# Kernel tuning notes

Measured on AMD Instinct MI355X. Metric: run time of the kernel, lower is better.

The kernel has to match this reference:

```python
import jax, jax.numpy as jnp
import numpy as np

B, IN_C, H, W = 2, 256, 128, 128
KQ = 128            # kq_dim
K_LOCAL = 5         # subsample_local_ksize -> 25 local samples
S = 32              # subsample_num_samples (25 local + 7 random global)
STRIDES = (1, 2, 4) # levels 2, 3, 4


def _local_inds(h, w, k):
    # create_local_ind_buffer: flat index of the KxK window around each pixel,
    # coordinates clamped at the border (padding by replication).
    off = np.arange(k) - k // 2
    ii = np.clip(np.arange(h)[:, None] + off[None, :], 0, h - 1)  # [h,k]
    jj = np.clip(np.arange(w)[:, None] + off[None, :], 0, w - 1)  # [w,k]
    inds = ii[:, None, :, None] * w + jj[None, :, None, :]        # [h,w,k,k]
    return inds.reshape(h * w, k * k)


def setup_inputs() -> dict:
    key = jax.random.key(0)
    ks = jax.random.split(key, 4)
    rng = np.random.RandomState(0)
    inp = {
        'feats': jax.random.normal(ks[0], (B, IN_C, H, W), jnp.float32),
        'conv_w': jax.random.normal(ks[1], (KQ, IN_C, 3, 3), jnp.float32) * 0.02,
        'conv_b': jnp.zeros((KQ,), jnp.float32),
        'key_w': jax.random.normal(ks[2], (KQ, KQ), jnp.float32) * 0.05,
        'key_b': jnp.zeros((KQ,), jnp.float32),
        'query_w': jax.random.normal(ks[3], (KQ, KQ), jnp.float32) * 0.05,
        'query_b': jnp.zeros((KQ,), jnp.float32),
    }
    for lvl, s in zip((2, 3, 4), STRIDES):
        h, w = H // s, W // s
        n = h * w
        loc = np.broadcast_to(_local_inds(h, w, K_LOCAL)[None], (B, n, K_LOCAL * K_LOCAL))
        glob = rng.randint(0, n, size=(B, n, S - K_LOCAL * K_LOCAL))
        inp['sample_inds_%d' % lvl] = jnp.asarray(np.concatenate([loc, glob], -1), jnp.int32)
    return inp


def _pool(x, s):
    # utils.downscale_tensor: average-pool by the level stride
    if s == 1:
        return x
    b, c, h, w = x.shape
    return x.reshape(b, c, h // s, s, w // s, s).mean(axis=(3, 5))


def _level_logits(key_f, query_f, stride, inds):
    k = _pool(key_f, stride)
    q = _pool(query_f, stride)
    b, c, h, w = k.shape
    k = k.reshape(b, c, h * w).transpose(0, 2, 1)   # [B,N,C]
    q = q.reshape(b, c, h * w).transpose(0, 2, 1)   # [B,N,C]
    gk = k[jnp.arange(b)[:, None, None], inds]      # gather keys -> [B,N,S,C]
    # (gathered_query * gathered_key).sum(-1); query gather at node_inds is identity
    return jnp.einsum('bnc,bnsc->bns', q, gk) * (c ** -0.5)


def reference(feats, conv_w, conv_b, key_w, key_b, query_w, query_b,
              sample_inds_2, sample_inds_3, sample_inds_4):
    x = jax.lax.conv_general_dilated(
        feats, conv_w, (1, 1), 'SAME',
        dimension_numbers=('NCHW', 'OIHW', 'NCHW')) + conv_b[None, :, None, None]
    keys = jnp.einsum('bchw,kc->bkhw', x, key_w) + key_b[None, :, None, None]
    queries = jnp.einsum('bchw,kc->bkhw', x, query_w) + query_b[None, :, None, None]
    logits = [
        _level_logits(keys, queries, s, i)
        for s, i in zip(STRIDES, (sample_inds_2, sample_inds_3, sample_inds_4))
    ]
    # subsample_logits for levels 2/3/4, concatenated along the node dim
    return jnp.concatenate(logits, axis=1)  # [B, 16384+4096+1024, S]
```

## Files before the change

kernel.cpp:

```cpp
#include <hip/hip_runtime.h>
#include <cstddef>
#include <cstdint>

typedef __attribute__((ext_vector_type(8))) short short8;
typedef __attribute__((ext_vector_type(4))) float f32x4;

namespace {
constexpr int B_   = 2;
constexpr int HW   = 16384;
constexpr int NTOT = 21504;
constexpr float SCALE = 0.088388347648318447f;
}

__device__ __forceinline__ unsigned short f2bf(float f) {
    unsigned u = __builtin_bit_cast(unsigned, f);
    u += 0x7fffu + ((u >> 16) & 1u);
    return (unsigned short)(u >> 16);
}
__device__ __forceinline__ float bf2f(unsigned short h) {
    return __builtin_bit_cast(float, (unsigned)h << 16);
}
__device__ __forceinline__ float blo(unsigned u) {
    return __builtin_bit_cast(float, u << 16);
}
__device__ __forceinline__ float bhi(unsigned u) {
    return __builtin_bit_cast(float, u & 0xffff0000u);
}
__device__ __forceinline__ unsigned pk2(float a, float b) {
    return (unsigned)f2bf(a) | ((unsigned)f2bf(b) << 16);
}
__device__ __forceinline__ void gload_lds16(const void* g, void* l) {
    __builtin_amdgcn_global_load_lds(
        (const __attribute__((address_space(1))) void*)g,
        (__attribute__((address_space(3))) void*)l, 16, 0, 0);
}

__global__ __launch_bounds__(256) void tp_k(
    const float* __restrict__ feats, const float* __restrict__ cw,
    const float* __restrict__ kw, const float* __restrict__ qw,
    const float* __restrict__ cb, const float* __restrict__ kb,
    const float* __restrict__ qb, unsigned short* __restrict__ fpm,
    unsigned short* __restrict__ wp, float* __restrict__ bias)
{
    const int bid = blockIdx.x;
    const int tid = threadIdx.x;

    if (bid < 520) {
        const int b = bid >= 260;
        const int rem = bid - b * 260;
        const int y = rem >> 1, xseg = rem & 1;
        const int lane = tid & 63, cg = tid >> 6;
        const int x = (xseg << 6) + lane;
        const bool inter = (y >= 1 && y <= 128);
        const float* src = feats + (((size_t)b * 256) << 14) + ((y - 1) << 7) + x;
        unsigned short* orow = fpm + ((size_t)(b * 130 + y) * 130 + 1 + x) * 256;

#pragma unroll
        for (int it = 0; it < 8; ++it) {
            const int c0 = (it << 5) + (cg << 3);
            uint4 v = {0u, 0u, 0u, 0u};
            if (inter) {
                float f0 = src[(size_t)(c0 + 0) << 14], f1 = src[(size_t)(c0 + 1) << 14];
                float f2 = src[(size_t)(c0 + 2) << 14], f3 = src[(size_t)(c0 + 3) << 14];
                float f4 = src[(size_t)(c0 + 4) << 14], f5 = src[(size_t)(c0 + 5) << 14];
                float f6 = src[(size_t)(c0 + 6) << 14], f7 = src[(size_t)(c0 + 7) << 14];
                v.x = pk2(f0, f1); v.y = pk2(f2, f3); v.z = pk2(f4, f5); v.w = pk2(f6, f7);
            }
            *(uint4*)(orow + c0) = v;
        }
        if (xseg == 0) {
            uint4 z = {0u, 0u, 0u, 0u};
            if (tid < 32)
                *(uint4*)(fpm + ((size_t)(b * 130 + y) * 130 + 0) * 256 + (tid << 3)) = z;
            else if (tid < 64)
                *(uint4*)(fpm + ((size_t)(b * 130 + y) * 130 + 129) * 256 + ((tid - 32) << 3)) = z;
        }
        return;
    }

    if (bid == 1096) {
        __shared__ float cbv[128];
        if (tid < 128) cbv[tid] = cb[tid];
        __syncthreads();
        const int oc = tid & 127, isQ = tid >> 7;
        const float* wrow = (isQ ? qw : kw) + oc * 128;
        float a = isQ ? qb[oc] : kb[oc];
        for (int j = 0; j < 128; ++j) a += wrow[j] * cbv[j];
        bias[tid] = a;
        return;
    }

    __shared__ float cvec[128][4];
    const int g = bid - 520;
    for (int idx = tid; idx < 512; idx += 256) {
        int j = idx >> 2, q = idx & 3;
        int pair = (g << 2) + q;
        int c = pair / 9, tap = pair - c * 9;
        cvec[j][q] = cw[j * 2304 + c * 9 + tap];
    }
    __syncthreads();
    const int oc = tid & 127, isQ = tid >> 7;
    const float* wrow = (isQ ? qw : kw) + oc * 128;
    float acc0 = 0.f, acc1 = 0.f, acc2 = 0.f, acc3 = 0.f;
    for (int j = 0; j < 128; ++j) {
        float wv = wrow[j];
        acc0 += wv * cvec[j][0]; acc1 += wv * cvec[j][1];
        acc2 += wv * cvec[j][2]; acc3 += wv * cvec[j][3];
    }
    float accs[4] = {acc0, acc1, acc2, acc3};
#pragma unroll
    for (int q = 0; q < 4; ++q) {
        int pair = (g << 2) + q;
        int c = pair / 9, tap = pair - c * 9;
        int chunk = c >> 5, kg = (c >> 3) & 3, i = c & 7;
        int nf = (isQ << 3) + (oc >> 4);
        int lane = (kg << 4) + (oc & 15);
        wp[((size_t)(((chunk * 9 + tap) << 4) + nf) << 9) + (lane << 3) + i] = f2bf(accs[q]);
    }
}

__global__ __launch_bounds__(256, 2) void conv3_k(
    const unsigned short* __restrict__ fpm, const unsigned short* __restrict__ wp,
    const float* __restrict__ kqbias, unsigned short* __restrict__ kT,
    unsigned short* __restrict__ qT, unsigned short* __restrict__ kT2,
    unsigned short* __restrict__ qT2, unsigned short* __restrict__ kT3,
    unsigned short* __restrict__ qT3)
{
    __shared__ __align__(16) unsigned char abuf[2][7168];
    __shared__ __align__(16) unsigned short obuf[64 * 264];

    const int tid = threadIdx.x;
    const int w = tid >> 6, lane = tid & 63;
    const int bid = blockIdx.x;
    const int b = bid >> 8, tile = bid & 255;
    const int ty0 = (tile >> 4) << 3, tx0 = (tile & 15) << 3;
    const int r = lane & 15, g = lane >> 4;

    const int sp_sub = lane >> 2, sp_o = (lane & 3) << 4;
    const int pbase = (((r >> 3) * 10) + (r & 7)) * 64 + (g << 4);
    const unsigned char* wpB = (const unsigned char*)wp + ((w << 2) << 10) + (lane << 4);

    f32x4 acc[4][4];
#pragma unroll
    for (int mi = 0; mi < 4; ++mi)
#pragma unroll
        for (int ni = 0; ni < 4; ++ni) acc[mi][ni] = (f32x4){0.f, 0.f, 0.f, 0.f};

    auto stage = [&](int chunk, int buf) {
#pragma unroll
        for (int k = 0; k < 2; ++k) {
            int i = w + (k << 2);
            if (i < 7) {
                int pl0 = (i << 4) + sp_sub;
                int y = (pl0 * 6554) >> 16;
                int x = pl0 - y * 10;
                const unsigned char* src = (const unsigned char*)fpm +
                    (((size_t)((b * 130 + ty0 + y) * 130 + tx0 + x)) << 9) +
                    (chunk << 6) + sp_o;
                gload_lds16(src, &abuf[buf][i << 10]);
            }
        }
    };

    stage(0, 0);
    __syncthreads();

    for (int chunk = 0; chunk < 8; ++chunk) {
        const unsigned char* ab = abuf[chunk & 1];
        if (chunk < 7) stage(chunk + 1, (chunk + 1) & 1);
        const unsigned char* wbase = wpB + (size_t)chunk * 147456;
#pragma unroll
        for (int tap = 0; tap < 9; ++tap) {
            const int dy = tap / 3, dx = tap % 3;
            short8 bf[4];
#pragma unroll
            for (int ni = 0; ni < 4; ++ni)
                bf[ni] = *(const short8*)(wbase + tap * 16384 + (ni << 10));
            short8 af[4];
#pragma unroll
            for (int mi = 0; mi < 4; ++mi)
                af[mi] = *(const short8*)(ab + pbase + (((2 * mi + dy) * 10 + dx) << 6));
#pragma unroll
            for (int mi = 0; mi < 4; ++mi)
#pragma unroll
                for (int ni = 0; ni < 4; ++ni)
                    acc[mi][ni] = __builtin_amdgcn_mfma_f32_16x16x32_bf16(
                        af[mi], bf[ni], acc[mi][ni], 0, 0, 0);
        }
        __syncthreads();
    }

    const int col = lane & 15;
    const int mrow0 = g << 2;
#pragma unroll
    for (int ni = 0; ni < 4; ++ni) {
        const int nf = (w << 2) + ni;
        const float bv = kqbias[(nf << 4) + col];
#pragma unroll
        for (int mi = 0; mi < 4; ++mi)
#pragma unroll
            for (int reg = 0; reg < 4; ++reg) {
                int m = mrow0 + reg;
                int pxl = ((2 * mi + (m >> 3)) << 3) + (m & 7);
                obuf[pxl * 264 + (nf << 4) + col] = f2bf(acc[mi][ni][reg] + bv);
            }
    }
    __syncthreads();

    {
        const int px = tid >> 2, q = tid & 3;
        const int gp = ((ty0 + (px >> 3)) << 7) + tx0 + (px & 7);
        const unsigned short* srow = obuf + px * 264 + (q << 6);
        unsigned short* dp = (q < 2)
            ? kT + ((((size_t)b << 14) + gp) << 7) + (q << 6)
            : qT + ((((size_t)b << 14) + gp) << 7) + ((q - 2) << 6);
#pragma unroll
        for (int j = 0; j < 8; ++j)
            *(uint4*)(dp + (j << 3)) = *(const uint4*)(srow + (j << 3));
    }

    {
        const int pp = tid >> 4, ocg = tid & 15, oc0 = ocg << 4;
        const int py2 = pp >> 2, px2 = pp & 3;
        const int gp2 = (((ty0 >> 1) + py2) << 6) + (tx0 >> 1) + px2;
        unsigned short* dp = (oc0 < 128)
            ? kT2 + (((size_t)b * 4096 + gp2) << 7) + oc0
            : qT2 + (((size_t)b * 4096 + gp2) << 7) + (oc0 - 128);
#pragma unroll
        for (int h = 0; h < 2; ++h) {
            float s0=0,s1=0,s2=0,s3=0,s4=0,s5=0,s6=0,s7=0;
#pragma unroll
            for (int dy = 0; dy < 2; ++dy)
#pragma unroll
                for (int dx = 0; dx < 2; ++dx) {
                    int pxl = (((py2 << 1) + dy) << 3) + (px2 << 1) + dx;
                    uint4 v = *(const uint4*)(obuf + pxl * 264 + oc0 + (h << 3));
                    s0 += blo(v.x); s1 += bhi(v.x); s2 += blo(v.y); s3 += bhi(v.y);
                    s4 += blo(v.z); s5 += bhi(v.z); s6 += blo(v.w); s7 += bhi(v.w);
                }
            uint4 o;
            o.x = pk2(s0 * 0.25f, s1 * 0.25f); o.y = pk2(s2 * 0.25f, s3 * 0.25f);
            o.z = pk2(s4 * 0.25f, s5 * 0.25f); o.w = pk2(s6 * 0.25f, s7 * 0.25f);
            *(uint4*)(dp + (h << 3)) = o;
        }
    }

    if (tid < 64) {
        const int pp = tid >> 4, ocg = tid & 15, oc0 = ocg << 4;
        const int py4 = pp >> 1, px4 = pp & 1;
        const int gp4 = (((ty0 >> 2) + py4) << 5) + (tx0 >> 2) + px4;
        unsigned short* dp = (oc0 < 128)
            ? kT3 + (((size_t)b * 1024 + gp4) << 7) + oc0
            : qT3 + (((size_t)b * 1024 + gp4) << 7) + (oc0 - 128);
#pragma unroll
        for (int h = 0; h < 2; ++h) {
            float s0=0,s1=0,s2=0,s3=0,s4=0,s5=0,s6=0,s7=0;
#pragma unroll
            for (int dy = 0; dy < 4; ++dy)
#pragma unroll
                for (int dx = 0; dx < 4; ++dx) {
                    int pxl = (((py4 << 2) + dy) << 3) + (px4 << 2) + dx;
                    uint4 v = *(const uint4*)(obuf + pxl * 264 + oc0 + (h << 3));
                    s0 += blo(v.x); s1 += bhi(v.x); s2 += blo(v.y); s3 += bhi(v.y);
                    s4 += blo(v.z); s5 += bhi(v.z); s6 += blo(v.w); s7 += bhi(v.w);
                }
            const float f = 0.0625f;
            uint4 o;
            o.x = pk2(s0 * f, s1 * f); o.y = pk2(s2 * f, s3 * f);
            o.z = pk2(s4 * f, s5 * f); o.w = pk2(s6 * f, s7 * f);
            *(uint4*)(dp + (h << 3)) = o;
        }
    }
}

__global__ __launch_bounds__(512) void gdot_all_k(
    const unsigned short* __restrict__ qT1, const unsigned short* __restrict__ kT1,
    const unsigned short* __restrict__ qT2, const unsigned short* __restrict__ kT2,
    const unsigned short* __restrict__ qT3, const unsigned short* __restrict__ kT3,
    const int* __restrict__ i2, const int* __restrict__ i3, const int* __restrict__ i4,
    float* __restrict__ out)
{
    __shared__ __align__(16) unsigned char kwin[144 * 256];

    const int raw = blockIdx.x;
    const int bid = (raw & 7) * 84 + (raw >> 3);

    const unsigned short *qT, *kT;
    const int* inds;
    int n, wshift, tpbsh, twsh, off;
    if (bid < 512) {
        qT = qT1; kT = kT1; inds = i2; n = 16384; wshift = 7; tpbsh = 8; twsh = 4; off = 0;
    } else if (bid < 640) {
        qT = qT2; kT = kT2; inds = i3; n = 4096;  wshift = 6; tpbsh = 6; twsh = 3; off = 16384;
    } else {
        qT = qT3; kT = kT3; inds = i4; n = 1024;  wshift = 5; tpbsh = 4; twsh = 2; off = 20480;
    }
    const int lb   = bid - ((bid < 512) ? 0 : (bid < 640) ? 512 : 640);
    const int b    = lb >> tpbsh;
    const int tile = lb & ((1 << tpbsh) - 1);
    const int ty0  = (tile >> twsh) << 3;
    const int tx0  = (tile & ((1 << twsh) - 1)) << 3;
    const int W    = 1 << wshift, Wm1 = W - 1;
    const int ry0  = ty0 - 2, cx0 = tx0 - 2;

    const int tid   = threadIdx.x;
    const int pxl   = tid >> 3;
    const int slice = tid & 7;
    const int py = pxl >> 3, px = pxl & 7;
    const int nid = ((ty0 + py) << wshift) + tx0 + px;

    for (int idx = tid; idx < 2304; idx += 512) {
        int slot = idx >> 4, w16 = idx & 15;
        int sy = ry0 + slot / 12, sx = cx0 + slot % 12;
        sy = min(max(sy, 0), Wm1); sx = min(max(sx, 0), Wm1);
        uint4 v = *(const uint4*)(kT + ((size_t)(b * n + (sy << wshift) + sx) * 128) + (w16 << 3));
        *(uint4*)&kwin[slot * 256 + ((w16 ^ (slot & 7)) << 4)] = v;
    }

    float qr[16];
    {
        const uint4* qp = (const uint4*)(qT + ((size_t)(b * n + nid) * 128) + (slice << 4));
        uint4 q0 = qp[0], q1 = qp[1];
        qr[0] = blo(q0.x); qr[1] = bhi(q0.x); qr[2] = blo(q0.y); qr[3] = bhi(q0.y);
        qr[4] = blo(q0.z); qr[5] = bhi(q0.z); qr[6] = blo(q0.w); qr[7] = bhi(q0.w);
        qr[8] = blo(q1.x); qr[9] = bhi(q1.x); qr[10] = blo(q1.y); qr[11] = bhi(q1.y);
        qr[12] = blo(q1.z); qr[13] = bhi(q1.z); qr[14] = blo(q1.w); qr[15] = bhi(q1.w);
    }
    __syncthreads();

    const int* irow = inds + ((size_t)(b * n + nid) << 5);
    int ia[32];
    {
        const int4* ip = (const int4*)irow;
#pragma unroll
        for (int j = 0; j < 8; ++j) {
            int4 v = ip[j];
            ia[4 * j] = v.x; ia[4 * j + 1] = v.y; ia[4 * j + 2] = v.z; ia[4 * j + 3] = v.w;
        }
    }

    uint4 rk0[7], rk1[7];
#pragma unroll
    for (int rr = 0; rr < 7; ++rr) {
        const uint4* kp = (const uint4*)(kT + (((size_t)(b * n + ia[25 + rr])) << 7) + (slice << 4));
        rk0[rr] = kp[0]; rk1[rr] = kp[1];
    }

    const int w2 = slice << 1;
    float res4[4] = {0.f, 0.f, 0.f, 0.f};
    float* orow = out + (((size_t)b * NTOT + off + nid) << 5);

#pragma unroll
    for (int s = 0; s < 32; ++s) {
        uint4 k0, k1;
        if (s < 25) {
            int ind = ia[s];
            int iy = ind >> wshift, ix = ind & Wm1;
            int slot = (iy - ry0) * 12 + (ix - cx0);
            int sw = slot & 7;
            const unsigned char* base2 = kwin + slot * 256;
            k0 = *(const uint4*)(base2 + ((w2 ^ sw) << 4));
            k1 = *(const uint4*)(base2 + (((w2 + 1) ^ sw) << 4));
        } else {
            k0 = rk0[s - 25]; k1 = rk1[s - 25];
        }
        float a = qr[0] * blo(k0.x) + qr[1] * bhi(k0.x)
                + qr[2] * blo(k0.y) + qr[3] * bhi(k0.y)
                + qr[4] * blo(k0.z) + qr[5] * bhi(k0.z)
                + qr[6] * blo(k0.w) + qr[7] * bhi(k0.w)
                + qr[8] * blo(k1.x) + qr[9] * bhi(k1.x)
                + qr[10] * blo(k1.y) + qr[11] * bhi(k1.y)
                + qr[12] * blo(k1.z) + qr[13] * bhi(k1.z)
                + qr[14] * blo(k1.w) + qr[15] * bhi(k1.w);
        a += __shfl_xor(a, 1);
        a += __shfl_xor(a, 2);
        a += __shfl_xor(a, 4);
        if ((s >> 2) == slice) res4[s & 3] = a * SCALE;
    }
    *(float4*)(orow + (slice << 2)) = *(const float4*)res4;
}

extern "C" void kernel_launch(void* const* d_in, const int* in_sizes, int n_in,
                              void* d_out, int out_size, void* d_ws, size_t ws_size,
                              hipStream_t stream)
{
    const float* feats = (const float*)d_in[0];
    const float* cw    = (const float*)d_in[1];
    const float* cb    = (const float*)d_in[2];
    const float* kw    = (const float*)d_in[3];
    const float* kb    = (const float*)d_in[4];
    const float* qw    = (const float*)d_in[5];
    const float* qb    = (const float*)d_in[6];
    const int*   i2    = (const int*)d_in[7];
    const int*   i3    = (const int*)d_in[8];
    const int*   i4    = (const int*)d_in[9];
    float* out = (float*)d_out;

    char* ws = (char*)d_ws;
    unsigned short* wp   = (unsigned short*)ws;
    float*          bias = (float*)(ws + 1179648);
    unsigned short* fpm  = (unsigned short*)(ws + 1180672);
    unsigned short* kT1  = (unsigned short*)(ws + 18624512);
    unsigned short* qT1  = kT1 + 4194304;
    unsigned short* kT2  = qT1 + 4194304;
    unsigned short* qT2  = kT2 + 1048576;
    unsigned short* kT3  = qT2 + 1048576;
    unsigned short* qT3  = kT3 + 262144;

    tp_k<<<dim3(1097), 256, 0, stream>>>(feats, cw, kw, qw, cb, kb, qb,
                                         fpm, wp, bias);
    conv3_k<<<dim3(512), 256, 0, stream>>>(fpm, wp, bias, kT1, qT1,
                                           kT2, qT2, kT3, qT3);
    gdot_all_k<<<dim3(672), 512, 0, stream>>>(qT1, kT1, qT2, kT2, qT3, kT3,
                                              i2, i3, i4, out);
}
```

Before: 181.2 us.

## Fuse three kernels into one cooperative persistent kernel with grid syncs

Merges the transpose/weight-prep, conv and gather-dot kernels into one cooperative kernel of 512 blocks that calls grid.sync() between phases. The aim is to remove launch gaps and inter-kernel drains. The gather-dot phase is also reworked from 512 to 256 threads, so each thread covers 32 channels and the random global keys are loaded inside the loop rather than prefetched. The costs are grid-sync overhead, occupancy limited to what a co-resident grid allows, and a less parallel gdot phase. If the cooperative launch fails, it falls back to three separate kernels.

```diff
diff --git a/kernel.cpp b/kernel.cpp
--- a/kernel.cpp
+++ b/kernel.cpp
@@ -1,6 +1,9 @@
 #include <hip/hip_runtime.h>
+#include <hip/hip_cooperative_groups.h>
 #include <cstddef>
 #include <cstdint>
+
+namespace cg = cooperative_groups;
 
 typedef __attribute__((ext_vector_type(8))) short short8;
 typedef __attribute__((ext_vector_type(4))) float f32x4;
@@ -35,21 +38,20 @@
         (__attribute__((address_space(3))) void*)l, 16, 0, 0);
 }
 
-__global__ __launch_bounds__(256) void tp_k(
+__device__ __forceinline__ void phase_tp(
+    int v, int tid,
     const float* __restrict__ feats, const float* __restrict__ cw,
     const float* __restrict__ kw, const float* __restrict__ qw,
     const float* __restrict__ cb, const float* __restrict__ kb,
     const float* __restrict__ qb, unsigned short* __restrict__ fpm,
-    unsigned short* __restrict__ wp, float* __restrict__ bias)
-{
-    const int bid = blockIdx.x;
-    const int tid = threadIdx.x;
-
-    if (bid < 520) {
-        const int b = bid >= 260;
-        const int rem = bid - b * 260;
+    unsigned short* __restrict__ wp, float* __restrict__ bias,
+    float* fsm)
+{
+    if (v < 520) {
+        const int b = v >= 260;
+        const int rem = v - b * 260;
         const int y = rem >> 1, xseg = rem & 1;
-        const int lane = tid & 63, cg = tid >> 6;
+        const int lane = tid & 63, cg2 = tid >> 6;
         const int x = (xseg << 6) + lane;
         const bool inter = (y >= 1 && y <= 128);
         const float* src = feats + (((size_t)b * 256) << 14) + ((y - 1) << 7) + x;
@@ -57,16 +59,16 @@
 
 #pragma unroll
         for (int it = 0; it < 8; ++it) {
-            const int c0 = (it << 5) + (cg << 3);
-            uint4 v = {0u, 0u, 0u, 0u};
+            const int c0 = (it << 5) + (cg2 << 3);
+            uint4 w = {0u, 0u, 0u, 0u};
             if (inter) {
                 float f0 = src[(size_t)(c0 + 0) << 14], f1 = src[(size_t)(c0 + 1) << 14];
                 float f2 = src[(size_t)(c0 + 2) << 14], f3 = src[(size_t)(c0 + 3) << 14];
                 float f4 = src[(size_t)(c0 + 4) << 14], f5 = src[(size_t)(c0 + 5) << 14];
                 float f6 = src[(size_t)(c0 + 6) << 14], f7 = src[(size_t)(c0 + 7) << 14];
-                v.x = pk2(f0, f1); v.y = pk2(f2, f3); v.z = pk2(f4, f5); v.w = pk2(f6, f7);
+                w.x = pk2(f0, f1); w.y = pk2(f2, f3); w.z = pk2(f4, f5); w.w = pk2(f6, f7);
             }
-            *(uint4*)(orow + c0) = v;
+            *(uint4*)(orow + c0) = w;
         }
         if (xseg == 0) {
             uint4 z = {0u, 0u, 0u, 0u};
@@ -78,8 +80,8 @@
         return;
     }
 
-    if (bid == 1096) {
-        __shared__ float cbv[128];
+    if (v == 1096) {
+        float* cbv = fsm;
         if (tid < 128) cbv[tid] = cb[tid];
         __syncthreads();
         const int oc = tid & 127, isQ = tid >> 7;
@@ -87,11 +89,12 @@
         float a = isQ ? qb[oc] : kb[oc];
         for (int j = 0; j < 128; ++j) a += wrow[j] * cbv[j];
         bias[tid] = a;
+        __syncthreads();
         return;
     }
 
-    __shared__ float cvec[128][4];
-    const int g = bid - 520;
+    float (*cvec)[4] = (float(*)[4])fsm;
+    const int g = v - 520;
     for (int idx = tid; idx < 512; idx += 256) {
         int j = idx >> 2, q = idx & 3;
         int pair = (g << 2) + q;
@@ -101,13 +104,13 @@
     __syncthreads();
     const int oc = tid & 127, isQ = tid >> 7;
     const float* wrow = (isQ ? qw : kw) + oc * 128;
-    float acc0 = 0.f, acc1 = 0.f, acc2 = 0.f, acc3 = 0.f;
+    float a0 = 0.f, a1 = 0.f, a2 = 0.f, a3 = 0.f;
     for (int j = 0; j < 128; ++j) {
         float wv = wrow[j];
-        acc0 += wv * cvec[j][0]; acc1 += wv * cvec[j][1];
-        acc2 += wv * cvec[j][2]; acc3 += wv * cvec[j][3];
-    }
-    float accs[4] = {acc0, acc1, acc2, acc3};
+        a0 += wv * cvec[j][0]; a1 += wv * cvec[j][1];
+        a2 += wv * cvec[j][2]; a3 += wv * cvec[j][3];
+    }
+    float accs[4] = {a0, a1, a2, a3};
 #pragma unroll
     for (int q = 0; q < 4; ++q) {
         int pair = (g << 2) + q;
@@ -117,21 +120,20 @@
         int lane = (kg << 4) + (oc & 15);
         wp[((size_t)(((chunk * 9 + tap) << 4) + nf) << 9) + (lane << 3) + i] = f2bf(accs[q]);
     }
-}
-
-__global__ __launch_bounds__(256, 2) void conv3_k(
+    __syncthreads();
+}
+
+__device__ __forceinline__ void phase_conv(
+    int bid, int tid,
     const unsigned short* __restrict__ fpm, const unsigned short* __restrict__ wp,
     const float* __restrict__ kqbias, unsigned short* __restrict__ kT,
     unsigned short* __restrict__ qT, unsigned short* __restrict__ kT2,
     unsigned short* __restrict__ qT2, unsigned short* __restrict__ kT3,
-    unsigned short* __restrict__ qT3)
-{
-    __shared__ __align__(16) unsigned char abuf[2][7168];
-    __shared__ __align__(16) unsigned short obuf[64 * 264];
-
-    const int tid = threadIdx.x;
+    unsigned short* __restrict__ qT3, unsigned char* smem)
+{
+    unsigned short* obuf = (unsigned short*)(smem + 14336);
+
     const int w = tid >> 6, lane = tid & 63;
-    const int bid = blockIdx.x;
     const int b = bid >> 8, tile = bid & 255;
     const int ty0 = (tile >> 4) << 3, tx0 = (tile & 15) << 3;
     const int r = lane & 15, g = lane >> 4;
@@ -157,7 +159,7 @@
                 const unsigned char* src = (const unsigned char*)fpm +
                     (((size_t)((b * 130 + ty0 + y) * 130 + tx0 + x)) << 9) +
                     (chunk << 6) + sp_o;
-                gload_lds16(src, &abuf[buf][i << 10]);
+                gload_lds16(src, smem + buf * 7168 + (i << 10));
             }
         }
     };
@@ -166,7 +168,7 @@
     __syncthreads();
 
     for (int chunk = 0; chunk < 8; ++chunk) {
-        const unsigned char* ab = abuf[chunk & 1];
+        const unsigned char* ab = smem + (chunk & 1) * 7168;
         if (chunk < 7) stage(chunk + 1, (chunk + 1) & 1);
         const unsigned char* wbase = wpB + (size_t)chunk * 147456;
 #pragma unroll
@@ -273,29 +275,25 @@
     }
 }
 
-__global__ __launch_bounds__(512) void gdot_all_k(
+__device__ __forceinline__ void phase_gdot(
+    int v, int tid,
     const unsigned short* __restrict__ qT1, const unsigned short* __restrict__ kT1,
     const unsigned short* __restrict__ qT2, const unsigned short* __restrict__ kT2,
     const unsigned short* __restrict__ qT3, const unsigned short* __restrict__ kT3,
     const int* __restrict__ i2, const int* __restrict__ i3, const int* __restrict__ i4,
-    float* __restrict__ out)
-{
-    __shared__ __align__(16) unsigned char kwin[144 * 256];
-
-    const int raw = blockIdx.x;
-    const int bid = (raw & 7) * 84 + (raw >> 3);
-
+    float* __restrict__ out, unsigned char* kwin)
+{
     const unsigned short *qT, *kT;
     const int* inds;
     int n, wshift, tpbsh, twsh, off;
-    if (bid < 512) {
+    if (v < 512) {
         qT = qT1; kT = kT1; inds = i2; n = 16384; wshift = 7; tpbsh = 8; twsh = 4; off = 0;
-    } else if (bid < 640) {
+    } else if (v < 640) {
         qT = qT2; kT = kT2; inds = i3; n = 4096;  wshift = 6; tpbsh = 6; twsh = 3; off = 16384;
     } else {
         qT = qT3; kT = kT3; inds = i4; n = 1024;  wshift = 5; tpbsh = 4; twsh = 2; off = 20480;
     }
-    const int lb   = bid - ((bid < 512) ? 0 : (bid < 640) ? 512 : 640);
+    const int lb   = v - ((v < 512) ? 0 : (v < 640) ? 512 : 640);
     const int b    = lb >> tpbsh;
     const int tile = lb & ((1 << tpbsh) - 1);
     const int ty0  = (tile >> twsh) << 3;
@@ -303,28 +301,31 @@
     const int W    = 1 << wshift, Wm1 = W - 1;
     const int ry0  = ty0 - 2, cx0 = tx0 - 2;
 
-    const int tid   = threadIdx.x;
-    const int pxl   = tid >> 3;
-    const int slice = tid & 7;
+    const int pxl = tid >> 2;
+    const int sl  = tid & 3;
     const int py = pxl >> 3, px = pxl & 7;
     const int nid = ((ty0 + py) << wshift) + tx0 + px;
 
-    for (int idx = tid; idx < 2304; idx += 512) {
+    for (int idx = tid; idx < 2304; idx += 256) {
         int slot = idx >> 4, w16 = idx & 15;
         int sy = ry0 + slot / 12, sx = cx0 + slot % 12;
         sy = min(max(sy, 0), Wm1); sx = min(max(sx, 0), Wm1);
-        uint4 v = *(const uint4*)(kT + ((size_t)(b * n + (sy << wshift) + sx) * 128) + (w16 << 3));
-        *(uint4*)&kwin[slot * 256 + ((w16 ^ (slot & 7)) << 4)] = v;
-    }
-
-    float qr[16];
+        uint4 vv = *(const uint4*)(kT + ((size_t)(b * n + (sy << wshift) + sx) << 7) + (w16 << 3));
+        *(uint4*)&kwin[slot * 256 + ((w16 ^ (slot & 7)) << 4)] = vv;
+    }
+
+    float qr[32];
     {
-        const uint4* qp = (const uint4*)(qT + ((size_t)(b * n + nid) * 128) + (slice << 4));
-        uint4 q0 = qp[0], q1 = qp[1];
-        qr[0] = blo(q0.x); qr[1] = bhi(q0.x); qr[2] = blo(q0.y); qr[3] = bhi(q0.y);
-        qr[4] = blo(q0.z); qr[5] = bhi(q0.z); qr[6] = blo(q0.w); qr[7] = bhi(q0.w);
-        qr[8] = blo(q1.x); qr[9] = bhi(q1.x); qr[10] = blo(q1.y); qr[11] = bhi(q1.y);
-        qr[12] = blo(q1.z); qr[13] = bhi(q1.z); qr[14] = blo(q1.w); qr[15] = bhi(q1.w);
+        const uint4* qp = (const uint4*)(qT + (((size_t)(b * n + nid)) << 7) + (sl << 5));
+        uint4 q0 = qp[0], q1 = qp[1], q2 = qp[2], q3 = qp[3];
+        qr[0]=blo(q0.x); qr[1]=bhi(q0.x); qr[2]=blo(q0.y); qr[3]=bhi(q0.y);
+        qr[4]=blo(q0.z); qr[5]=bhi(q0.z); qr[6]=blo(q0.w); qr[7]=bhi(q0.w);
+        qr[8]=blo(q1.x); qr[9]=bhi(q1.x); qr[10]=blo(q1.y); qr[11]=bhi(q1.y);
+        qr[12]=blo(q1.z); qr[13]=bhi(q1.z); qr[14]=blo(q1.w); qr[15]=bhi(q1.w);
+        qr[16]=blo(q2.x); qr[17]=bhi(q2.x); qr[18]=blo(q2.y); qr[19]=bhi(q2.y);
+        qr[20]=blo(q2.z); qr[21]=bhi(q2.z); qr[22]=blo(q2.w); qr[23]=bhi(q2.w);
+        qr[24]=blo(q3.x); qr[25]=bhi(q3.x); qr[26]=blo(q3.y); qr[27]=bhi(q3.y);
+        qr[28]=blo(q3.z); qr[29]=bhi(q3.z); qr[30]=blo(q3.w); qr[31]=bhi(q3.w);
     }
     __syncthreads();
 
@@ -334,50 +335,102 @@
         const int4* ip = (const int4*)irow;
 #pragma unroll
         for (int j = 0; j < 8; ++j) {
-            int4 v = ip[j];
-            ia[4 * j] = v.x; ia[4 * j + 1] = v.y; ia[4 * j + 2] = v.z; ia[4 * j + 3] = v.w;
-        }
-    }
-
-    uint4 rk0[7], rk1[7];
-#pragma unroll
-    for (int rr = 0; rr < 7; ++rr) {
-        const uint4* kp = (const uint4*)(kT + (((size_t)(b * n + ia[25 + rr])) << 7) + (slice << 4));
-        rk0[rr] = kp[0]; rk1[rr] = kp[1];
-    }
-
-    const int w2 = slice << 1;
-    float res4[4] = {0.f, 0.f, 0.f, 0.f};
+            int4 t = ip[j];
+            ia[4*j] = t.x; ia[4*j+1] = t.y; ia[4*j+2] = t.z; ia[4*j+3] = t.w;
+        }
+    }
+
+    const int w16b = sl << 2;
+    float res[8];
     float* orow = out + (((size_t)b * NTOT + off + nid) << 5);
 
 #pragma unroll
     for (int s = 0; s < 32; ++s) {
-        uint4 k0, k1;
+        uint4 k0, k1, k2, k3;
         if (s < 25) {
             int ind = ia[s];
             int iy = ind >> wshift, ix = ind & Wm1;
             int slot = (iy - ry0) * 12 + (ix - cx0);
             int sw = slot & 7;
             const unsigned char* base2 = kwin + slot * 256;
-            k0 = *(const uint4*)(base2 + ((w2 ^ sw) << 4));
-            k1 = *(const uint4*)(base2 + (((w2 + 1) ^ sw) << 4));
+            k0 = *(const uint4*)(base2 + (((w16b + 0) ^ sw) << 4));
+            k1 = *(const uint4*)(base2 + (((w16b + 1) ^ sw) << 4));
+            k2 = *(const uint4*)(base2 + (((w16b + 2) ^ sw) << 4));
+            k3 = *(const uint4*)(base2 + (((w16b + 3) ^ sw) << 4));
         } else {
-            k0 = rk0[s - 25]; k1 = rk1[s - 25];
-        }
-        float a = qr[0] * blo(k0.x) + qr[1] * bhi(k0.x)
-                + qr[2] * blo(k0.y) + qr[3] * bhi(k0.y)
-                + qr[4] * blo(k0.z) + qr[5] * bhi(k0.z)
-                + qr[6] * blo(k0.w) + qr[7] * bhi(k0.w)
-                + qr[8] * blo(k1.x) + qr[9] * bhi(k1.x)
-                + qr[10] * blo(k1.y) + qr[11] * bhi(k1.y)
-                + qr[12] * blo(k1.z) + qr[13] * bhi(k1.z)
-                + qr[14] * blo(k1.w) + qr[15] * bhi(k1.w);
+            const uint4* kp = (const uint4*)(kT + (((size_t)(b * n + ia[s])) << 7) + (sl << 5));
+            k0 = kp[0]; k1 = kp[1]; k2 = kp[2]; k3 = kp[3];
+        }
+        float a = qr[0]*blo(k0.x) + qr[1]*bhi(k0.x) + qr[2]*blo(k0.y) + qr[3]*bhi(k0.y)
+                + qr[4]*blo(k0.z) + qr[5]*bhi(k0.z) + qr[6]*blo(k0.w) + qr[7]*bhi(k0.w)
+                + qr[8]*blo(k1.x) + qr[9]*bhi(k1.x) + qr[10]*blo(k1.y) + qr[11]*bhi(k1.y)
+                + qr[12]*blo(k1.z) + qr[13]*bhi(k1.z) + qr[14]*blo(k1.w) + qr[15]*bhi(k1.w)
+                + qr[16]*blo(k2.x) + qr[17]*bhi(k2.x) + qr[18]*blo(k2.y) + qr[19]*bhi(k2.y)
+                + qr[20]*blo(k2.z) + qr[21]*bhi(k2.z) + qr[22]*blo(k2.w) + qr[23]*bhi(k2.w)
+                + qr[24]*blo(k3.x) + qr[25]*bhi(k3.x) + qr[26]*blo(k3.y) + qr[27]*bhi(k3.y)
+                + qr[28]*blo(k3.z) + qr[29]*bhi(k3.z) + qr[30]*blo(k3.w) + qr[31]*bhi(k3.w);
         a += __shfl_xor(a, 1);
         a += __shfl_xor(a, 2);
-        a += __shfl_xor(a, 4);
-        if ((s >> 2) == slice) res4[s & 3] = a * SCALE;
-    }
-    *(float4*)(orow + (slice << 2)) = *(const float4*)res4;
+        if ((s >> 3) == sl) res[s & 7] = a * SCALE;
+    }
+    float4 r0 = {res[0], res[1], res[2], res[3]};
+    float4 r1 = {res[4], res[5], res[6], res[7]};
+    *(float4*)(orow + (sl << 3)) = r0;
+    *(float4*)(orow + (sl << 3) + 4) = r1;
+    __syncthreads();
+}
+
+__global__ __launch_bounds__(256, 2) void fused_k(
+    const float* feats, const float* cw, const float* kw, const float* qw,
+    const float* cb, const float* kb, const float* qb,
+    unsigned short* fpm, unsigned short* wp, float* bias,
+    unsigned short* kT1, unsigned short* qT1, unsigned short* kT2,
+    unsigned short* qT2, unsigned short* kT3, unsigned short* qT3,
+    const int* i2, const int* i3, const int* i4, float* out)
+{
+    __shared__ __align__(16) unsigned char smem[48128];
+    const int tid = threadIdx.x;
+    cg::grid_group grid = cg::this_grid();
+
+    for (int v = blockIdx.x; v < 1097; v += 512)
+        phase_tp(v, tid, feats, cw, kw, qw, cb, kb, qb, fpm, wp, bias, (float*)smem);
+
+    grid.sync();
+
+    phase_conv(blockIdx.x, tid, fpm, wp, bias, kT1, qT1, kT2, qT2, kT3, qT3, smem);
+
+    grid.sync();
+
+    for (int v = blockIdx.x; v < 672; v += 512)
+        phase_gdot(v, tid, qT1, kT1, qT2, kT2, qT3, kT3, i2, i3, i4, out, smem);
+}
+
+__global__ __launch_bounds__(256) void tp_sep_k(
+    const float* feats, const float* cw, const float* kw, const float* qw,
+    const float* cb, const float* kb, const float* qb,
+    unsigned short* fpm, unsigned short* wp, float* bias)
+{
+    __shared__ __align__(16) float fsm[512];
+    phase_tp(blockIdx.x, threadIdx.x, feats, cw, kw, qw, cb, kb, qb, fpm, wp, bias, fsm);
+}
+
+__global__ __launch_bounds__(256, 2) void conv_sep_k(
+    const unsigned short* fpm, const unsigned short* wp, const float* kqbias,
+    unsigned short* kT1, unsigned short* qT1, unsigned short* kT2,
+    unsigned short* qT2, unsigned short* kT3, unsigned short* qT3)
+{
+    __shared__ __align__(16) unsigned char smem[48128];
+    phase_conv(blockIdx.x, threadIdx.x, fpm, wp, kqbias, kT1, qT1, kT2, qT2, kT3, qT3, smem);
+}
+
+__global__ __launch_bounds__(256) void gdot_sep_k(
+    const unsigned short* qT1, const unsigned short* kT1,
+    const unsigned short* qT2, const unsigned short* kT2,
+    const unsigned short* qT3, const unsigned short* kT3,
+    const int* i2, const int* i3, const int* i4, float* out)
+{
+    __shared__ __align__(16) unsigned char kwin[36864];
+    phase_gdot(blockIdx.x, threadIdx.x, qT1, kT1, qT2, kT2, qT3, kT3, i2, i3, i4, out, kwin);
 }
 
 extern "C" void kernel_launch(void* const* d_in, const int* in_sizes, int n_in,
@@ -407,10 +460,23 @@
     unsigned short* kT3  = qT2 + 1048576;
     unsigned short* qT3  = kT3 + 262144;
 
-    tp_k<<<dim3(1097), 256, 0, stream>>>(feats, cw, kw, qw, cb, kb, qb,
-                                         fpm, wp, bias);
-    conv3_k<<<dim3(512), 256, 0, stream>>>(fpm, wp, bias, kT1, qT1,
-                                           kT2, qT2, kT3, qT3);
-    gdot_all_k<<<dim3(672), 512, 0, stream>>>(qT1, kT1, qT2, kT2, qT3, kT3,
-                                              i2, i3, i4, out);
-}
+    void* args[] = {
+        (void*)&feats, (void*)&cw, (void*)&kw, (void*)&qw,
+        (void*)&cb, (void*)&kb, (void*)&qb,
+        (void*)&fpm, (void*)&wp, (void*)&bias,
+        (void*)&kT1, (void*)&qT1, (void*)&kT2, (void*)&qT2,
+        (void*)&kT3, (void*)&qT3,
+        (void*)&i2, (void*)&i3, (void*)&i4, (void*)&out
+    };
+    hipError_t err = hipLaunchCooperativeKernel(
+        (const void*)fused_k, dim3(512), dim3(256), args, 0, stream);
+
+    if (err != hipSuccess) {
+        tp_sep_k<<<dim3(1097), 256, 0, stream>>>(feats, cw, kw, qw, cb, kb, qb,
+                                                 fpm, wp, bias);
+        conv_sep_k<<<dim3(512), 256, 0, stream>>>(fpm, wp, bias, kT1, qT1,
+                                                  kT2, qT2, kT3, qT3);
+        gdot_sep_k<<<dim3(672), 256, 0, stream>>>(qT1, kT1, qT2, kT2, qT3, kT3,
+                                                  i2, i3, i4, out);
+    }
+}
```

After: 342.8 us. 1.89x slower.

## Split fused conv GEMM across output-channel halves to double block count

Applied to the files above, without the earlier changes.

The fused conv+key/query projection kernel is split so each block computes only the key or the query half (128 output channels) for its 8x8 pixel tile, launching 1024 blocks instead of 512. Per-wave accumulators halve, the output staging buffer shrinks, and the launch bound asks for 4 blocks per CU, all aimed at higher occupancy and better CU fill. In exchange, every input tile is staged from global memory twice, once per half.

```diff
diff --git a/kernel.cpp b/kernel.cpp
--- a/kernel.cpp
+++ b/kernel.cpp
@@ -101,13 +101,13 @@
     __syncthreads();
     const int oc = tid & 127, isQ = tid >> 7;
     const float* wrow = (isQ ? qw : kw) + oc * 128;
-    float acc0 = 0.f, acc1 = 0.f, acc2 = 0.f, acc3 = 0.f;
+    float a0 = 0.f, a1 = 0.f, a2 = 0.f, a3 = 0.f;
     for (int j = 0; j < 128; ++j) {
         float wv = wrow[j];
-        acc0 += wv * cvec[j][0]; acc1 += wv * cvec[j][1];
-        acc2 += wv * cvec[j][2]; acc3 += wv * cvec[j][3];
-    }
-    float accs[4] = {acc0, acc1, acc2, acc3};
+        a0 += wv * cvec[j][0]; a1 += wv * cvec[j][1];
+        a2 += wv * cvec[j][2]; a3 += wv * cvec[j][3];
+    }
+    float accs[4] = {a0, a1, a2, a3};
 #pragma unroll
     for (int q = 0; q < 4; ++q) {
         int pair = (g << 2) + q;
@@ -119,7 +119,7 @@
     }
 }
 
-__global__ __launch_bounds__(256, 2) void conv3_k(
+__global__ __launch_bounds__(256, 4) void conv5_k(
     const unsigned short* __restrict__ fpm, const unsigned short* __restrict__ wp,
     const float* __restrict__ kqbias, unsigned short* __restrict__ kT,
     unsigned short* __restrict__ qT, unsigned short* __restrict__ kT2,
@@ -127,24 +127,27 @@
     unsigned short* __restrict__ qT3)
 {
     __shared__ __align__(16) unsigned char abuf[2][7168];
-    __shared__ __align__(16) unsigned short obuf[64 * 264];
+    __shared__ __align__(16) unsigned short obuf[64 * 136];
 
     const int tid = threadIdx.x;
     const int w = tid >> 6, lane = tid & 63;
     const int bid = blockIdx.x;
-    const int b = bid >> 8, tile = bid & 255;
+    const int h = bid & 1;
+    const int t = bid >> 1;
+    const int b = t >> 8, tile = t & 255;
     const int ty0 = (tile >> 4) << 3, tx0 = (tile & 15) << 3;
     const int r = lane & 15, g = lane >> 4;
 
     const int sp_sub = lane >> 2, sp_o = (lane & 3) << 4;
     const int pbase = (((r >> 3) * 10) + (r & 7)) * 64 + (g << 4);
-    const unsigned char* wpB = (const unsigned char*)wp + ((w << 2) << 10) + (lane << 4);
-
-    f32x4 acc[4][4];
+    const unsigned char* wpB = (const unsigned char*)wp +
+        (((h << 3) + (w << 1)) << 10) + (lane << 4);
+
+    f32x4 acc[4][2];
 #pragma unroll
     for (int mi = 0; mi < 4; ++mi)
 #pragma unroll
-        for (int ni = 0; ni < 4; ++ni) acc[mi][ni] = (f32x4){0.f, 0.f, 0.f, 0.f};
+        for (int ni = 0; ni < 2; ++ni) acc[mi][ni] = (f32x4){0.f, 0.f, 0.f, 0.f};
 
     auto stage = [&](int chunk, int buf) {
 #pragma unroll
@@ -172,9 +175,9 @@
 #pragma unroll
         for (int tap = 0; tap < 9; ++tap) {
             const int dy = tap / 3, dx = tap % 3;
-            short8 bf[4];
-#pragma unroll
-            for (int ni = 0; ni < 4; ++ni)
+            short8 bf[2];
+#pragma unroll
+            for (int ni = 0; ni < 2; ++ni)
                 bf[ni] = *(const short8*)(wbase + tap * 16384 + (ni << 10));
             short8 af[4];
 #pragma unroll
@@ -183,7 +186,7 @@
 #pragma unroll
             for (int mi = 0; mi < 4; ++mi)
 #pragma unroll
-                for (int ni = 0; ni < 4; ++ni)
+                for (int ni = 0; ni < 2; ++ni)
                     acc[mi][ni] = __builtin_amdgcn_mfma_f32_16x16x32_bf16(
                         af[mi], bf[ni], acc[mi][ni], 0, 0, 0);
         }
@@ -193,83 +196,75 @@
     const int col = lane & 15;
     const int mrow0 = g << 2;
 #pragma unroll
-    for (int ni = 0; ni < 4; ++ni) {
-        const int nf = (w << 2) + ni;
-        const float bv = kqbias[(nf << 4) + col];
+    for (int ni = 0; ni < 2; ++ni) {
+        const int nf_loc = (w << 1) + ni;
+        const float bv = kqbias[(h << 7) + (nf_loc << 4) + col];
 #pragma unroll
         for (int mi = 0; mi < 4; ++mi)
 #pragma unroll
             for (int reg = 0; reg < 4; ++reg) {
                 int m = mrow0 + reg;
                 int pxl = ((2 * mi + (m >> 3)) << 3) + (m & 7);
-                obuf[pxl * 264 + (nf << 4) + col] = f2bf(acc[mi][ni][reg] + bv);
+                obuf[pxl * 136 + (nf_loc << 4) + col] = f2bf(acc[mi][ni][reg] + bv);
             }
     }
     __syncthreads();
+
+    unsigned short* dst1 = h ? qT : kT;
+    unsigned short* dst2 = h ? qT2 : kT2;
+    unsigned short* dst3 = h ? qT3 : kT3;
 
     {
         const int px = tid >> 2, q = tid & 3;
         const int gp = ((ty0 + (px >> 3)) << 7) + tx0 + (px & 7);
-        const unsigned short* srow = obuf + px * 264 + (q << 6);
-        unsigned short* dp = (q < 2)
-            ? kT + ((((size_t)b << 14) + gp) << 7) + (q << 6)
-            : qT + ((((size_t)b << 14) + gp) << 7) + ((q - 2) << 6);
-#pragma unroll
-        for (int j = 0; j < 8; ++j)
+        const unsigned short* srow = obuf + px * 136 + (q << 5);
+        unsigned short* dp = dst1 + ((((size_t)b << 14) + gp) << 7) + (q << 5);
+#pragma unroll
+        for (int j = 0; j < 4; ++j)
             *(uint4*)(dp + (j << 3)) = *(const uint4*)(srow + (j << 3));
     }
 
     {
-        const int pp = tid >> 4, ocg = tid & 15, oc0 = ocg << 4;
+        const int pp = tid >> 4, ocg = tid & 15, oc0 = ocg << 3;
         const int py2 = pp >> 2, px2 = pp & 3;
         const int gp2 = (((ty0 >> 1) + py2) << 6) + (tx0 >> 1) + px2;
-        unsigned short* dp = (oc0 < 128)
-            ? kT2 + (((size_t)b * 4096 + gp2) << 7) + oc0
-            : qT2 + (((size_t)b * 4096 + gp2) << 7) + (oc0 - 128);
-#pragma unroll
-        for (int h = 0; h < 2; ++h) {
-            float s0=0,s1=0,s2=0,s3=0,s4=0,s5=0,s6=0,s7=0;
-#pragma unroll
-            for (int dy = 0; dy < 2; ++dy)
-#pragma unroll
-                for (int dx = 0; dx < 2; ++dx) {
-                    int pxl = (((py2 << 1) + dy) << 3) + (px2 << 1) + dx;
-                    uint4 v = *(const uint4*)(obuf + pxl * 264 + oc0 + (h << 3));
-                    s0 += blo(v.x); s1 += bhi(v.x); s2 += blo(v.y); s3 += bhi(v.y);
-                    s4 += blo(v.z); s5 += bhi(v.z); s6 += blo(v.w); s7 += bhi(v.w);
-                }
-            uint4 o;
-            o.x = pk2(s0 * 0.25f, s1 * 0.25f); o.y = pk2(s2 * 0.25f, s3 * 0.25f);
-            o.z = pk2(s4 * 0.25f, s5 * 0.25f); o.w = pk2(s6 * 0.25f, s7 * 0.25f);
-            *(uint4*)(dp + (h << 3)) = o;
-        }
+        unsigned short* dp = dst2 + (((size_t)b * 4096 + gp2) << 7) + oc0;
+        float s0=0,s1=0,s2=0,s3=0,s4=0,s5=0,s6=0,s7=0;
+#pragma unroll
+        for (int dy = 0; dy < 2; ++dy)
+#pragma unroll
+            for (int dx = 0; dx < 2; ++dx) {
+                int pxl = (((py2 << 1) + dy) << 3) + (px2 << 1) + dx;
+                uint4 v = *(const uint4*)(obuf + pxl * 136 + oc0);
+                s0 += blo(v.x); s1 += bhi(v.x); s2 += blo(v.y); s3 += bhi(v.y);
+                s4 += blo(v.z); s5 += bhi(v.z); s6 += blo(v.w); s7 += bhi(v.w);
+            }
+        uint4 o;
+        o.x = pk2(s0 * 0.25f, s1 * 0.25f); o.y = pk2(s2 * 0.25f, s3 * 0.25f);
+        o.z = pk2(s4 * 0.25f, s5 * 0.25f); o.w = pk2(s6 * 0.25f, s7 * 0.25f);
+        *(uint4*)dp = o;
     }
 
     if (tid < 64) {
-        const int pp = tid >> 4, ocg = tid & 15, oc0 = ocg << 4;
+        const int pp = tid >> 4, ocg = tid & 15, oc0 = ocg << 3;
         const int py4 = pp >> 1, px4 = pp & 1;
         const int gp4 = (((ty0 >> 2) + py4) << 5) + (tx0 >> 2) + px4;
-        unsigned short* dp = (oc0 < 128)
-            ? kT3 + (((size_t)b * 1024 + gp4) << 7) + oc0
-            : qT3 + (((size_t)b * 1024 + gp4) << 7) + (oc0 - 128);
-#pragma unroll
-        for (int h = 0; h < 2; ++h) {
-            float s0=0,s1=0,s2=0,s3=0,s4=0,s5=0,s6=0,s7=0;
-#pragma unroll
-            for (int dy = 0; dy < 4; ++dy)
-#pragma unroll
-                for (int dx = 0; dx < 4; ++dx) {
-                    int pxl = (((py4 << 2) + dy) << 3) + (px4 << 2) + dx;
-                    uint4 v = *(const uint4*)(obuf + pxl * 264 + oc0 + (h << 3));
-                    s0 += blo(v.x); s1 += bhi(v.x); s2 += blo(v.y); s3 += bhi(v.y);
-                    s4 += blo(v.z); s5 += bhi(v.z); s6 += blo(v.w); s7 += bhi(v.w);
-                }
-            const float f = 0.0625f;
-            uint4 o;
-            o.x = pk2(s0 * f, s1 * f); o.y = pk2(s2 * f, s3 * f);
-            o.z = pk2(s4 * f, s5 * f); o.w = pk2(s6 * f, s7 * f);
-            *(uint4*)(dp + (h << 3)) = o;
-        }
+        unsigned short* dp = dst3 + (((size_t)b * 1024 + gp4) << 7) + oc0;
+        float s0=0,s1=0,s2=0,s3=0,s4=0,s5=0,s6=0,s7=0;
+#pragma unroll
+        for (int dy = 0; dy < 4; ++dy)
+#pragma unroll
+            for (int dx = 0; dx < 4; ++dx) {
+                int pxl = (((py4 << 2) + dy) << 3) + (px4 << 2) + dx;
+                uint4 v = *(const uint4*)(obuf + pxl * 136 + oc0);
+                s0 += blo(v.x); s1 += bhi(v.x); s2 += blo(v.y); s3 += bhi(v.y);
+                s4 += blo(v.z); s5 += bhi(v.z); s6 += blo(v.w); s7 += bhi(v.w);
+            }
+        const float f = 0.0625f;
+        uint4 o;
+        o.x = pk2(s0 * f, s1 * f); o.y = pk2(s2 * f, s3 * f);
+        o.z = pk2(s4 * f, s5 * f); o.w = pk2(s6 * f, s7 * f);
+        *(uint4*)dp = o;
     }
 }
 
@@ -409,8 +404,8 @@
 
     tp_k<<<dim3(1097), 256, 0, stream>>>(feats, cw, kw, qw, cb, kb, qb,
                                          fpm, wp, bias);
-    conv3_k<<<dim3(512), 256, 0, stream>>>(fpm, wp, bias, kT1, qT1,
-                                           kT2, qT2, kT3, qT3);
+    conv5_k<<<dim3(1024), 256, 0, stream>>>(fpm, wp, bias, kT1, qT1,
+                                            kT2, qT2, kT3, qT3);
     gdot_all_k<<<dim3(672), 512, 0, stream>>>(qT1, kT1, qT2, kT2, qT3, kT3,
                                               i2, i3, i4, out);
 }
```

Result: faster. 176.6 us (-2.6%).
